# Performance work log

Measured on AMD Instinct MI355X. Metric: run time of the kernel, lower is better.

The kernel has to match this reference:

```python
import jax, jax.numpy as jnp
import numpy as np

NUM_Q = 8
B, N, D = 8, 1024, 512
C = 1024


def setup_inputs() -> dict:
    key = jax.random.key(0)
    k1, k2 = jax.random.split(key)
    x = jax.random.normal(k1, (B, N, D), dtype=jnp.float32)
    codebooks = jax.random.normal(k2, (NUM_Q, C, D), dtype=jnp.float32)
    return {"x": x, "codebooks": codebooks}


def _vq_layer(residual, codebook):
    # residual: [b, n, d]; codebook: [c, d]
    # squared euclidean distances without materializing differences tensor
    r2 = jnp.sum(residual * residual, axis=-1, keepdims=True)          # [b, n, 1]
    e2 = jnp.sum(codebook * codebook, axis=-1)                          # [c]
    dots = jnp.einsum('bnd,cd->bnc', residual, codebook)                # [b, n, c]
    dist = r2 - 2.0 * dots + e2                                         # [b, n, c]
    indices = jnp.argmin(dist, axis=-1)                                 # [b, n] int32
    quantized = codebook[indices]                                       # [b, n, d]
    # straight-through estimator (codebook is EMA-updated, not differentiated)
    quantized_st = residual + jax.lax.stop_gradient(quantized - residual)
    # commitment loss (default commitment_weight = 1.0)
    loss = jnp.mean((jax.lax.stop_gradient(quantized_st) - residual) ** 2)
    return quantized_st, indices, loss


def reference(x, codebooks):
    def step(carry, codebook):
        residual, quantized_out = carry
        quantized, indices, loss = _vq_layer(residual, codebook)
        return (residual - quantized, quantized_out + quantized), (indices, loss)

    init = (x, jnp.zeros_like(x))
    (_, quantized_out), (all_indices, all_losses) = jax.lax.scan(step, init, codebooks)
    # all_indices: [q, b, n] -> [b, n, q]; all_losses: [q]
    all_indices = jnp.transpose(all_indices, (1, 2, 0))
    return quantized_out, all_indices, all_losses
```

## Files before the change

kernel.cpp:

```cpp
#include <hip/hip_runtime.h>
#include <float.h>

#define NUM_Q 8
#define BN    8192
#define D     512
#define C     1024

#define QOUT_OFF 0
#define IDX_OFF  (BN * D)
#define LOSS_OFF (IDX_OFF + BN * NUM_Q)

#define WIN_OFF_B  0
#define E2_OFF_B   (BN * 8)

typedef _Float16 f16x8 __attribute__((ext_vector_type(8)));
typedef float    f32x4 __attribute__((ext_vector_type(4)));

#define TM  128
#define TN  128
#define BKK 32
#define LDK 40
#define GTHREADS 512

__device__ __forceinline__ unsigned fkey(float f) {
    unsigned u = __float_as_uint(f);
    return (u & 0x80000000u) ? ~u : (u | 0x80000000u);
}

__device__ __forceinline__ unsigned long long u64min(unsigned long long a, unsigned long long b) {
    return a < b ? a : b;
}

__device__ __forceinline__ unsigned long long shfl_xor_u64(unsigned long long v, int m) {
    int lo = __shfl_xor((int)(unsigned)v, m, 64);
    int hi = __shfl_xor((int)(unsigned)(v >> 32), m, 64);
    return ((unsigned long long)(unsigned)hi << 32) | (unsigned)lo;
}

__global__ void rvq_init_kernel(const float* __restrict__ x, float* __restrict__ out,
                                unsigned long long* __restrict__ winners) {
    int i = blockIdx.x * blockDim.x + threadIdx.x;
    const float4* x4 = (const float4*)x;
    float4* r4 = (float4*)(out + QOUT_OFF);
    const int n4 = BN * D / 4;
    for (int k = i; k < n4; k += gridDim.x * blockDim.x)
        r4[k] = x4[k];
    if (i < BN) winners[i] = ~0ull;
    if (i < NUM_Q) out[LOSS_OFF + i] = 0.0f;
}

__global__ void rvq_e2_kernel(const float* __restrict__ cbs, float* __restrict__ e2ws) {
    const int row = blockIdx.x;
    const int lane = threadIdx.x;
    const float* p = cbs + (size_t)row * D + lane * 8;
    float4 a = *(const float4*)p;
    float4 b = *(const float4*)(p + 4);
    float ss = a.x*a.x + a.y*a.y + a.z*a.z + a.w*a.w
             + b.x*b.x + b.y*b.y + b.z*b.z + b.w*b.w;
#pragma unroll
    for (int off = 32; off >= 1; off >>= 1) ss += __shfl_xor(ss, off, 64);
    if (lane == 0) e2ws[row] = ss;
}

__global__ __launch_bounds__(GTHREADS, 4) void rvq_score_kernel(
    const float* __restrict__ cb,
    const float* __restrict__ R,
    const float* __restrict__ e2,
    unsigned long long* __restrict__ winners)
{
    __shared__ __align__(16) _Float16 AsHi[TM][LDK];
    __shared__ __align__(16) _Float16 AsLo[TM][LDK];
    __shared__ __align__(16) _Float16 BsHi[TN][LDK];
    __shared__ __align__(16) _Float16 BsLo[TN][LDK];
    __shared__ unsigned long long part[4][TM];

    const int tid  = threadIdx.x;
    const int lane = tid & 63;
    const int wv   = tid >> 6;
    const int wm   = wv & 1;
    const int wn   = wv >> 1;
    const int lm   = lane & 15;
    const int lq   = lane >> 4;

    const int mg = blockIdx.x & 63;
    const int nb = blockIdx.x >> 6;
    const int tok0 = mg * TM;
    const int cb0  = nb * TN;

    const int srow = tid >> 2;
    const int skq  = tid & 3;

    const float* Ag = R  + (size_t)(tok0 + srow) * D + skq * 8;
    const float* Bg = cb + (size_t)(cb0  + srow) * D + skq * 8;

    f32x4 acc[4][2];
#pragma unroll
    for (int mt = 0; mt < 4; ++mt)
#pragma unroll
        for (int nt = 0; nt < 2; ++nt)
            acc[mt][nt] = (f32x4){0.f, 0.f, 0.f, 0.f};

    for (int kb = 0; kb < D / BKK; ++kb) {
        const int kc = kb * BKK;
        float4 a0 = *(const float4*)(Ag + kc);
        float4 a1 = *(const float4*)(Ag + kc + 4);
        float4 b0 = *(const float4*)(Bg + kc);
        float4 b1 = *(const float4*)(Bg + kc + 4);

        __syncthreads();

        {
            float av[8] = {a0.x, a0.y, a0.z, a0.w, a1.x, a1.y, a1.z, a1.w};
            f16x8 h, l;
#pragma unroll
            for (int i = 0; i < 8; ++i) {
                _Float16 hi = (_Float16)av[i];
                h[i] = hi;
                l[i] = (_Float16)(av[i] - (float)hi);
            }
            *(f16x8*)&AsHi[srow][skq * 8] = h;
            *(f16x8*)&AsLo[srow][skq * 8] = l;
        }
        {
            float bv[8] = {b0.x, b0.y, b0.z, b0.w, b1.x, b1.y, b1.z, b1.w};
            f16x8 h, l;
#pragma unroll
            for (int i = 0; i < 8; ++i) {
                _Float16 hi = (_Float16)bv[i];
                h[i] = hi;
                l[i] = (_Float16)(bv[i] - (float)hi);
            }
            *(f16x8*)&BsHi[srow][skq * 8] = h;
            *(f16x8*)&BsLo[srow][skq * 8] = l;
        }
        __syncthreads();

        f16x8 ah[4], al[4], bh[2], bl[2];
#pragma unroll
        for (int mt = 0; mt < 4; ++mt) {
            ah[mt] = *(const f16x8*)&AsHi[wm * 64 + mt * 16 + lm][lq * 8];
            al[mt] = *(const f16x8*)&AsLo[wm * 64 + mt * 16 + lm][lq * 8];
        }
#pragma unroll
        for (int nt = 0; nt < 2; ++nt) {
            bh[nt] = *(const f16x8*)&BsHi[wn * 32 + nt * 16 + lm][lq * 8];
            bl[nt] = *(const f16x8*)&BsLo[wn * 32 + nt * 16 + lm][lq * 8];
        }
#pragma unroll
        for (int mt = 0; mt < 4; ++mt)
#pragma unroll
            for (int nt = 0; nt < 2; ++nt)
                acc[mt][nt] = __builtin_amdgcn_mfma_f32_16x16x32_f16(ah[mt], bh[nt], acc[mt][nt], 0, 0, 0);
#pragma unroll
        for (int mt = 0; mt < 4; ++mt)
#pragma unroll
            for (int nt = 0; nt < 2; ++nt)
                acc[mt][nt] = __builtin_amdgcn_mfma_f32_16x16x32_f16(ah[mt], bl[nt], acc[mt][nt], 0, 0, 0);
#pragma unroll
        for (int mt = 0; mt < 4; ++mt)
#pragma unroll
            for (int nt = 0; nt < 2; ++nt)
                acc[mt][nt] = __builtin_amdgcn_mfma_f32_16x16x32_f16(al[mt], bh[nt], acc[mt][nt], 0, 0, 0);
    }

    const int n0 = cb0 + wn * 32 + lm;
    const float e2v0 = e2[n0];
    const float e2v1 = e2[n0 + 16];

#pragma unroll
    for (int mt = 0; mt < 4; ++mt) {
#pragma unroll
        for (int r = 0; r < 4; ++r) {
            float s0 = e2v0 - 2.0f * acc[mt][0][r];
            float s1 = e2v1 - 2.0f * acc[mt][1][r];
            unsigned long long p0 = ((unsigned long long)fkey(s0) << 32) | (unsigned)n0;
            unsigned long long p1 = ((unsigned long long)fkey(s1) << 32) | (unsigned)(n0 + 16);
            unsigned long long p = u64min(p0, p1);
#pragma unroll
            for (int off = 1; off < 16; off <<= 1)
                p = u64min(p, shfl_xor_u64(p, off));
            if (lm == 0)
                part[wn][wm * 64 + mt * 16 + lq * 4 + r] = p;
        }
    }
    __syncthreads();
    if (tid < TM) {
        unsigned long long p = part[0][tid];
        p = u64min(p, part[1][tid]);
        p = u64min(p, part[2][tid]);
        p = u64min(p, part[3][tid]);
        atomicMin(&winners[tok0 + tid], p);
    }
}

__global__ __launch_bounds__(256) void rvq_update_kernel(
    const float* __restrict__ cb, float* __restrict__ out,
    unsigned long long* __restrict__ winners, int q)
{
    __shared__ float lsum[4];
    const int tid = threadIdx.x;
    const int tl  = tid >> 4;
    const int g   = tid & 15;
    const int tok = blockIdx.x * 16 + tl;

    float* R = out + QOUT_OFF;
    unsigned long long w = winners[tok];
    const int best = (int)(unsigned)(w & 0xFFFFFFFFull);
    const float* crow = cb + (size_t)best * D;
    float* rrow = R + (size_t)tok * D;

    float ss = 0.0f;
#pragma unroll
    for (int m = 0; m < 8; ++m) {
        const int off = (m * 16 + g) * 4;
        float4 r = *(const float4*)&rrow[off];
        float4 c = *(const float4*)&crow[off];
        float4 nr = make_float4(r.x - c.x, r.y - c.y, r.z - c.z, r.w - c.w);
        *(float4*)&rrow[off] = nr;
        ss += nr.x * nr.x + nr.y * nr.y + nr.z * nr.z + nr.w * nr.w;
    }
    if (g == 0) {
        out[IDX_OFF + (size_t)tok * NUM_Q + q] = (float)best;
        winners[tok] = ~0ull;
    }
#pragma unroll
    for (int off = 32; off >= 1; off >>= 1) ss += __shfl_xor(ss, off, 64);
    if ((tid & 63) == 0) lsum[tid >> 6] = ss;
    __syncthreads();
    if (tid == 0)
        atomicAdd(out + LOSS_OFF + q, lsum[0] + lsum[1] + lsum[2] + lsum[3]);
}

__global__ void rvq_finalize_kernel(const float* __restrict__ x, float* __restrict__ out) {
    int i = blockIdx.x * blockDim.x + threadIdx.x;
    const float4* x4 = (const float4*)x;
    float4* o4 = (float4*)(out + QOUT_OFF);
    const int n4 = BN * D / 4;
    for (int k = i; k < n4; k += gridDim.x * blockDim.x) {
        float4 xv = x4[k];
        float4 rv = o4[k];
        o4[k] = make_float4(xv.x - rv.x, xv.y - rv.y, xv.z - rv.z, xv.w - rv.w);
    }
    if (i < NUM_Q) out[LOSS_OFF + i] *= (1.0f / (float)(BN * D));
}

extern "C" void kernel_launch(void* const* d_in, const int* in_sizes, int n_in,
                              void* d_out, int out_size, void* d_ws, size_t ws_size,
                              hipStream_t stream) {
    const float* x   = (const float*)d_in[0];
    const float* cbs = (const float*)d_in[1];
    float* out = (float*)d_out;
    unsigned long long* winners = (unsigned long long*)((char*)d_ws + WIN_OFF_B);
    float* e2ws = (float*)((char*)d_ws + E2_OFF_B);

    hipLaunchKernelGGL(rvq_init_kernel, dim3(1024), dim3(256), 0, stream, x, out, winners);
    hipLaunchKernelGGL(rvq_e2_kernel, dim3(NUM_Q * C), dim3(64), 0, stream, cbs, e2ws);

    float* R = out + QOUT_OFF;
    for (int q = 0; q < NUM_Q; ++q) {
        const float* cb_q = cbs + (size_t)q * C * D;
        hipLaunchKernelGGL(rvq_score_kernel, dim3((BN / TM) * (C / TN)), dim3(GTHREADS), 0, stream,
                           cb_q, R, e2ws + (size_t)q * C, winners);
        hipLaunchKernelGGL(rvq_update_kernel, dim3(BN / 16), dim3(256), 0, stream,
                           cb_q, out, winners, q);
    }
    hipLaunchKernelGGL(rvq_finalize_kernel, dim3(1024), dim3(256), 0, stream, x, out);
}
```

Baseline: 445.3 us.

## Fuse all quantizer stages into one persistent per-token-block kernel with pre-split codebooks

Replaces the per-stage score/update kernel pairs with a single kernel. Each block owns 32 tokens, keeps their residuals in registers across all eight stages, and computes the full 1024-code argmin locally, so no global winners array or atomics are needed. The codebooks are split once into fp16 hi/lo halves by a prep kernel and read straight from global or L2 by MFMA fragments, which removes per-tile conversion and the residual round-trips through memory. Only 256 blocks of 512 threads run, so GPU occupancy is lower and each block re-reads the whole codebook every stage, making L2 bandwidth the likely limit.

New measurement: 644.8 us. 1.45x slower.

```diff
diff --git a/kernel.cpp b/kernel.cpp
--- a/kernel.cpp
+++ b/kernel.cpp
@@ -1,5 +1,4 @@
 #include <hip/hip_runtime.h>
-#include <float.h>
 
 #define NUM_Q 8
 #define BN    8192
@@ -10,238 +9,202 @@
 #define IDX_OFF  (BN * D)
 #define LOSS_OFF (IDX_OFF + BN * NUM_Q)
 
-#define WIN_OFF_B  0
-#define E2_OFF_B   (BN * 8)
+#define CBP_OFF_B 0
+#define E2_OFF_B  (NUM_Q * C * 1024 * 2)
 
 typedef _Float16 f16x8 __attribute__((ext_vector_type(8)));
+typedef _Float16 f16x4 __attribute__((ext_vector_type(4)));
 typedef float    f32x4 __attribute__((ext_vector_type(4)));
-
-#define TM  128
-#define TN  128
-#define BKK 32
-#define LDK 40
-#define GTHREADS 512
 
 __device__ __forceinline__ unsigned fkey(float f) {
     unsigned u = __float_as_uint(f);
     return (u & 0x80000000u) ? ~u : (u | 0x80000000u);
 }
-
 __device__ __forceinline__ unsigned long long u64min(unsigned long long a, unsigned long long b) {
     return a < b ? a : b;
 }
-
 __device__ __forceinline__ unsigned long long shfl_xor_u64(unsigned long long v, int m) {
     int lo = __shfl_xor((int)(unsigned)v, m, 64);
     int hi = __shfl_xor((int)(unsigned)(v >> 32), m, 64);
     return ((unsigned long long)(unsigned)hi << 32) | (unsigned)lo;
 }
 
-__global__ void rvq_init_kernel(const float* __restrict__ x, float* __restrict__ out,
-                                unsigned long long* __restrict__ winners) {
-    int i = blockIdx.x * blockDim.x + threadIdx.x;
-    const float4* x4 = (const float4*)x;
-    float4* r4 = (float4*)(out + QOUT_OFF);
-    const int n4 = BN * D / 4;
-    for (int k = i; k < n4; k += gridDim.x * blockDim.x)
-        r4[k] = x4[k];
-    if (i < BN) winners[i] = ~0ull;
-    if (i < NUM_Q) out[LOSS_OFF + i] = 0.0f;
-}
-
-__global__ void rvq_e2_kernel(const float* __restrict__ cbs, float* __restrict__ e2ws) {
-    const int row = blockIdx.x;
-    const int lane = threadIdx.x;
+__global__ __launch_bounds__(256) void rvq_prep(const float* __restrict__ cbs,
+                                                _Float16* __restrict__ cbp,
+                                                float* __restrict__ e2ws,
+                                                float* __restrict__ out) {
+    const int row  = blockIdx.x * 4 + (threadIdx.x >> 6);
+    const int lane = threadIdx.x & 63;
     const float* p = cbs + (size_t)row * D + lane * 8;
     float4 a = *(const float4*)p;
     float4 b = *(const float4*)(p + 4);
-    float ss = a.x*a.x + a.y*a.y + a.z*a.z + a.w*a.w
-             + b.x*b.x + b.y*b.y + b.z*b.z + b.w*b.w;
+    float av[8] = {a.x, a.y, a.z, a.w, b.x, b.y, b.z, b.w};
+    f16x8 h, l;
+    float ss = 0.f;
+#pragma unroll
+    for (int i = 0; i < 8; ++i) {
+        _Float16 hi = (_Float16)av[i];
+        h[i] = hi;
+        l[i] = (_Float16)(av[i] - (float)hi);
+        ss += av[i] * av[i];
+    }
+    _Float16* dst = cbp + (size_t)row * 1024;
+    *(f16x8*)(dst + lane * 8)       = h;
+    *(f16x8*)(dst + 512 + lane * 8) = l;
 #pragma unroll
     for (int off = 32; off >= 1; off >>= 1) ss += __shfl_xor(ss, off, 64);
     if (lane == 0) e2ws[row] = ss;
-}
-
-__global__ __launch_bounds__(GTHREADS, 4) void rvq_score_kernel(
-    const float* __restrict__ cb,
-    const float* __restrict__ R,
-    const float* __restrict__ e2,
-    unsigned long long* __restrict__ winners)
+    if (blockIdx.x == 0 && threadIdx.x < NUM_Q) out[LOSS_OFF + threadIdx.x] = 0.0f;
+}
+
+__global__ __launch_bounds__(512, 2) void rvq_fused(
+    const float* __restrict__ x, const float* __restrict__ cbs,
+    const _Float16* __restrict__ cbp, const float* __restrict__ e2ws,
+    float* __restrict__ out)
 {
-    __shared__ __align__(16) _Float16 AsHi[TM][LDK];
-    __shared__ __align__(16) _Float16 AsLo[TM][LDK];
-    __shared__ __align__(16) _Float16 BsHi[TN][LDK];
-    __shared__ __align__(16) _Float16 BsLo[TN][LDK];
-    __shared__ unsigned long long part[4][TM];
+    __shared__ __align__(16) unsigned char smem[65536];
 
     const int tid  = threadIdx.x;
     const int lane = tid & 63;
     const int wv   = tid >> 6;
-    const int wm   = wv & 1;
-    const int wn   = wv >> 1;
     const int lm   = lane & 15;
     const int lq   = lane >> 4;
-
-    const int mg = blockIdx.x & 63;
-    const int nb = blockIdx.x >> 6;
-    const int tok0 = mg * TM;
-    const int cb0  = nb * TN;
-
-    const int srow = tid >> 2;
-    const int skq  = tid & 3;
-
-    const float* Ag = R  + (size_t)(tok0 + srow) * D + skq * 8;
-    const float* Bg = cb + (size_t)(cb0  + srow) * D + skq * 8;
-
-    f32x4 acc[4][2];
-#pragma unroll
-    for (int mt = 0; mt < 4; ++mt)
-#pragma unroll
-        for (int nt = 0; nt < 2; ++nt)
-            acc[mt][nt] = (f32x4){0.f, 0.f, 0.f, 0.f};
-
-    for (int kb = 0; kb < D / BKK; ++kb) {
-        const int kc = kb * BKK;
-        float4 a0 = *(const float4*)(Ag + kc);
-        float4 a1 = *(const float4*)(Ag + kc + 4);
-        float4 b0 = *(const float4*)(Bg + kc);
-        float4 b1 = *(const float4*)(Bg + kc + 4);
-
-        __syncthreads();
-
-        {
-            float av[8] = {a0.x, a0.y, a0.z, a0.w, a1.x, a1.y, a1.z, a1.w};
-            f16x8 h, l;
-#pragma unroll
-            for (int i = 0; i < 8; ++i) {
-                _Float16 hi = (_Float16)av[i];
-                h[i] = hi;
-                l[i] = (_Float16)(av[i] - (float)hi);
+    const int tl   = tid >> 4;
+    const int g    = tid & 15;
+    const int tok0 = blockIdx.x * 32;
+
+    auto aab = [](int row, int kbyte) -> unsigned {
+        return (((unsigned)row << 10) + (unsigned)kbyte) ^ (unsigned)((row & 7) << 4);
+    };
+
+    float4 r4[8];
+    {
+        const float* xr = x + (size_t)(tok0 + tl) * D + g * 4;
+#pragma unroll
+        for (int j = 0; j < 8; ++j) r4[j] = *(const float4*)(xr + j * 64);
+    }
+
+    unsigned long long* red = (unsigned long long*)smem;
+
+    for (int q = 0; q < NUM_Q; ++q) {
+#pragma unroll
+        for (int j = 0; j < 8; ++j) {
+            float4 v = r4[j];
+            f16x4 h, l;
+            h[0] = (_Float16)v.x; l[0] = (_Float16)(v.x - (float)h[0]);
+            h[1] = (_Float16)v.y; l[1] = (_Float16)(v.y - (float)h[1]);
+            h[2] = (_Float16)v.z; l[2] = (_Float16)(v.z - (float)h[2]);
+            h[3] = (_Float16)v.w; l[3] = (_Float16)(v.w - (float)h[3]);
+            unsigned b = aab(tl, (g * 4 + j * 64) * 2);
+            *(f16x4*)(smem + b)         = h;
+            *(f16x4*)(smem + 32768 + b) = l;
+        }
+        __syncthreads();
+
+        const _Float16* bp[8];
+#pragma unroll
+        for (int nt = 0; nt < 8; ++nt)
+            bp[nt] = cbp + (((size_t)(q * C + wv * 128 + nt * 16 + lm)) << 10) + lq * 8;
+
+        f32x4 acc[2][8];
+#pragma unroll
+        for (int mt = 0; mt < 2; ++mt)
+#pragma unroll
+            for (int nt = 0; nt < 8; ++nt)
+                acc[mt][nt] = (f32x4){0.f, 0.f, 0.f, 0.f};
+
+#pragma unroll
+        for (int kb = 0; kb < 16; ++kb) {
+            unsigned b0 = aab(lm,      kb * 64 + lq * 16);
+            unsigned b1 = aab(16 + lm, kb * 64 + lq * 16);
+            f16x8 ah0 = *(const f16x8*)(smem + b0);
+            f16x8 ah1 = *(const f16x8*)(smem + b1);
+            f16x8 al0 = *(const f16x8*)(smem + 32768 + b0);
+            f16x8 al1 = *(const f16x8*)(smem + 32768 + b1);
+#pragma unroll
+            for (int nt = 0; nt < 8; ++nt) {
+                f16x8 bh = *(const f16x8*)(bp[nt] + kb * 32);
+                f16x8 bl = *(const f16x8*)(bp[nt] + 512 + kb * 32);
+                acc[0][nt] = __builtin_amdgcn_mfma_f32_16x16x32_f16(ah0, bh, acc[0][nt], 0, 0, 0);
+                acc[1][nt] = __builtin_amdgcn_mfma_f32_16x16x32_f16(ah1, bh, acc[1][nt], 0, 0, 0);
+                acc[0][nt] = __builtin_amdgcn_mfma_f32_16x16x32_f16(ah0, bl, acc[0][nt], 0, 0, 0);
+                acc[1][nt] = __builtin_amdgcn_mfma_f32_16x16x32_f16(ah1, bl, acc[1][nt], 0, 0, 0);
+                acc[0][nt] = __builtin_amdgcn_mfma_f32_16x16x32_f16(al0, bh, acc[0][nt], 0, 0, 0);
+                acc[1][nt] = __builtin_amdgcn_mfma_f32_16x16x32_f16(al1, bh, acc[1][nt], 0, 0, 0);
             }
-            *(f16x8*)&AsHi[srow][skq * 8] = h;
-            *(f16x8*)&AsLo[srow][skq * 8] = l;
-        }
-        {
-            float bv[8] = {b0.x, b0.y, b0.z, b0.w, b1.x, b1.y, b1.z, b1.w};
-            f16x8 h, l;
-#pragma unroll
-            for (int i = 0; i < 8; ++i) {
-                _Float16 hi = (_Float16)bv[i];
-                h[i] = hi;
-                l[i] = (_Float16)(bv[i] - (float)hi);
+        }
+        __syncthreads();
+
+        const float* e2q = e2ws + q * C;
+        float e2v[8];
+#pragma unroll
+        for (int nt = 0; nt < 8; ++nt) e2v[nt] = e2q[wv * 128 + nt * 16 + lm];
+
+        unsigned long long best[2][4];
+#pragma unroll
+        for (int mt = 0; mt < 2; ++mt)
+#pragma unroll
+            for (int r = 0; r < 4; ++r) best[mt][r] = ~0ull;
+
+#pragma unroll
+        for (int mt = 0; mt < 2; ++mt)
+#pragma unroll
+            for (int nt = 0; nt < 8; ++nt) {
+                unsigned col = (unsigned)(wv * 128 + nt * 16 + lm);
+#pragma unroll
+                for (int r = 0; r < 4; ++r) {
+                    float s = e2v[nt] - 2.0f * acc[mt][nt][r];
+                    unsigned long long p = ((unsigned long long)fkey(s) << 32) | col;
+                    best[mt][r] = u64min(best[mt][r], p);
+                }
             }
-            *(f16x8*)&BsHi[srow][skq * 8] = h;
-            *(f16x8*)&BsLo[srow][skq * 8] = l;
-        }
-        __syncthreads();
-
-        f16x8 ah[4], al[4], bh[2], bl[2];
-#pragma unroll
-        for (int mt = 0; mt < 4; ++mt) {
-            ah[mt] = *(const f16x8*)&AsHi[wm * 64 + mt * 16 + lm][lq * 8];
-            al[mt] = *(const f16x8*)&AsLo[wm * 64 + mt * 16 + lm][lq * 8];
-        }
-#pragma unroll
-        for (int nt = 0; nt < 2; ++nt) {
-            bh[nt] = *(const f16x8*)&BsHi[wn * 32 + nt * 16 + lm][lq * 8];
-            bl[nt] = *(const f16x8*)&BsLo[wn * 32 + nt * 16 + lm][lq * 8];
-        }
-#pragma unroll
-        for (int mt = 0; mt < 4; ++mt)
-#pragma unroll
-            for (int nt = 0; nt < 2; ++nt)
-                acc[mt][nt] = __builtin_amdgcn_mfma_f32_16x16x32_f16(ah[mt], bh[nt], acc[mt][nt], 0, 0, 0);
-#pragma unroll
-        for (int mt = 0; mt < 4; ++mt)
-#pragma unroll
-            for (int nt = 0; nt < 2; ++nt)
-                acc[mt][nt] = __builtin_amdgcn_mfma_f32_16x16x32_f16(ah[mt], bl[nt], acc[mt][nt], 0, 0, 0);
-#pragma unroll
-        for (int mt = 0; mt < 4; ++mt)
-#pragma unroll
-            for (int nt = 0; nt < 2; ++nt)
-                acc[mt][nt] = __builtin_amdgcn_mfma_f32_16x16x32_f16(al[mt], bh[nt], acc[mt][nt], 0, 0, 0);
-    }
-
-    const int n0 = cb0 + wn * 32 + lm;
-    const float e2v0 = e2[n0];
-    const float e2v1 = e2[n0 + 16];
-
-#pragma unroll
-    for (int mt = 0; mt < 4; ++mt) {
-#pragma unroll
-        for (int r = 0; r < 4; ++r) {
-            float s0 = e2v0 - 2.0f * acc[mt][0][r];
-            float s1 = e2v1 - 2.0f * acc[mt][1][r];
-            unsigned long long p0 = ((unsigned long long)fkey(s0) << 32) | (unsigned)n0;
-            unsigned long long p1 = ((unsigned long long)fkey(s1) << 32) | (unsigned)(n0 + 16);
-            unsigned long long p = u64min(p0, p1);
-#pragma unroll
-            for (int off = 1; off < 16; off <<= 1)
-                p = u64min(p, shfl_xor_u64(p, off));
-            if (lm == 0)
-                part[wn][wm * 64 + mt * 16 + lq * 4 + r] = p;
-        }
-    }
-    __syncthreads();
-    if (tid < TM) {
-        unsigned long long p = part[0][tid];
-        p = u64min(p, part[1][tid]);
-        p = u64min(p, part[2][tid]);
-        p = u64min(p, part[3][tid]);
-        atomicMin(&winners[tok0 + tid], p);
-    }
-}
-
-__global__ __launch_bounds__(256) void rvq_update_kernel(
-    const float* __restrict__ cb, float* __restrict__ out,
-    unsigned long long* __restrict__ winners, int q)
-{
-    __shared__ float lsum[4];
-    const int tid = threadIdx.x;
-    const int tl  = tid >> 4;
-    const int g   = tid & 15;
-    const int tok = blockIdx.x * 16 + tl;
-
-    float* R = out + QOUT_OFF;
-    unsigned long long w = winners[tok];
-    const int best = (int)(unsigned)(w & 0xFFFFFFFFull);
-    const float* crow = cb + (size_t)best * D;
-    float* rrow = R + (size_t)tok * D;
-
-    float ss = 0.0f;
-#pragma unroll
-    for (int m = 0; m < 8; ++m) {
-        const int off = (m * 16 + g) * 4;
-        float4 r = *(const float4*)&rrow[off];
-        float4 c = *(const float4*)&crow[off];
-        float4 nr = make_float4(r.x - c.x, r.y - c.y, r.z - c.z, r.w - c.w);
-        *(float4*)&rrow[off] = nr;
-        ss += nr.x * nr.x + nr.y * nr.y + nr.z * nr.z + nr.w * nr.w;
-    }
-    if (g == 0) {
-        out[IDX_OFF + (size_t)tok * NUM_Q + q] = (float)best;
-        winners[tok] = ~0ull;
-    }
-#pragma unroll
-    for (int off = 32; off >= 1; off >>= 1) ss += __shfl_xor(ss, off, 64);
-    if ((tid & 63) == 0) lsum[tid >> 6] = ss;
-    __syncthreads();
-    if (tid == 0)
-        atomicAdd(out + LOSS_OFF + q, lsum[0] + lsum[1] + lsum[2] + lsum[3]);
-}
-
-__global__ void rvq_finalize_kernel(const float* __restrict__ x, float* __restrict__ out) {
-    int i = blockIdx.x * blockDim.x + threadIdx.x;
-    const float4* x4 = (const float4*)x;
-    float4* o4 = (float4*)(out + QOUT_OFF);
-    const int n4 = BN * D / 4;
-    for (int k = i; k < n4; k += gridDim.x * blockDim.x) {
-        float4 xv = x4[k];
-        float4 rv = o4[k];
-        o4[k] = make_float4(xv.x - rv.x, xv.y - rv.y, xv.z - rv.z, xv.w - rv.w);
-    }
-    if (i < NUM_Q) out[LOSS_OFF + i] *= (1.0f / (float)(BN * D));
+#pragma unroll
+        for (int mt = 0; mt < 2; ++mt)
+#pragma unroll
+            for (int r = 0; r < 4; ++r) {
+#pragma unroll
+                for (int off = 1; off < 16; off <<= 1)
+                    best[mt][r] = u64min(best[mt][r], shfl_xor_u64(best[mt][r], off));
+                if (lm == 0) red[wv * 32 + mt * 16 + lq * 4 + r] = best[mt][r];
+            }
+        __syncthreads();
+        if (tid < 32) {
+            unsigned long long p = red[tid];
+#pragma unroll
+            for (int w = 1; w < 8; ++w) p = u64min(p, red[w * 32 + tid]);
+            red[tid] = p;
+        }
+        __syncthreads();
+        const unsigned bidx = (unsigned)(red[tl] & 0xffffffffull);
+
+        const float* cw = cbs + ((size_t)q * C + bidx) * D + g * 4;
+        float ss = 0.f;
+#pragma unroll
+        for (int j = 0; j < 8; ++j) {
+            float4 c = *(const float4*)(cw + j * 64);
+            float4 v = r4[j];
+            v.x -= c.x; v.y -= c.y; v.z -= c.z; v.w -= c.w;
+            r4[j] = v;
+            ss += v.x * v.x + v.y * v.y + v.z * v.z + v.w * v.w;
+        }
+        if (g == 0) out[IDX_OFF + (size_t)(tok0 + tl) * NUM_Q + q] = (float)bidx;
+#pragma unroll
+        for (int off = 32; off >= 1; off >>= 1) ss += __shfl_xor(ss, off, 64);
+        if (lane == 0) atomicAdd(out + LOSS_OFF + q, ss * (1.0f / ((float)BN * (float)D)));
+        __syncthreads();
+    }
+
+    {
+        const float* xr = x + (size_t)(tok0 + tl) * D + g * 4;
+        float* qo = out + QOUT_OFF + (size_t)(tok0 + tl) * D + g * 4;
+#pragma unroll
+        for (int j = 0; j < 8; ++j) {
+            float4 xv = *(const float4*)(xr + j * 64);
+            float4 v  = r4[j];
+            *(float4*)(qo + j * 64) =
+                make_float4(xv.x - v.x, xv.y - v.y, xv.z - v.z, xv.w - v.w);
+        }
+    }
 }
 
 extern "C" void kernel_launch(void* const* d_in, const int* in_sizes, int n_in,
@@ -250,19 +213,9 @@
     const float* x   = (const float*)d_in[0];
     const float* cbs = (const float*)d_in[1];
     float* out = (float*)d_out;
-    unsigned long long* winners = (unsigned long long*)((char*)d_ws + WIN_OFF_B);
-    float* e2ws = (float*)((char*)d_ws + E2_OFF_B);
-
-    hipLaunchKernelGGL(rvq_init_kernel, dim3(1024), dim3(256), 0, stream, x, out, winners);
-    hipLaunchKernelGGL(rvq_e2_kernel, dim3(NUM_Q * C), dim3(64), 0, stream, cbs, e2ws);
-
-    float* R = out + QOUT_OFF;
-    for (int q = 0; q < NUM_Q; ++q) {
-        const float* cb_q = cbs + (size_t)q * C * D;
-        hipLaunchKernelGGL(rvq_score_kernel, dim3((BN / TM) * (C / TN)), dim3(GTHREADS), 0, stream,
-                           cb_q, R, e2ws + (size_t)q * C, winners);
-        hipLaunchKernelGGL(rvq_update_kernel, dim3(BN / 16), dim3(256), 0, stream,
-                           cb_q, out, winners, q);
-    }
-    hipLaunchKernelGGL(rvq_finalize_kernel, dim3(1024), dim3(256), 0, stream, x, out);
-}
+    _Float16* cbp = (_Float16*)((char*)d_ws + CBP_OFF_B);
+    float* e2ws   = (float*)((char*)d_ws + E2_OFF_B);
+
+    hipLaunchKernelGGL(rvq_prep,  dim3(NUM_Q * C / 4), dim3(256), 0, stream, cbs, cbp, e2ws, out);
+    hipLaunchKernelGGL(rvq_fused, dim3(BN / 32),       dim3(512), 0, stream, x, cbs, cbp, e2ws, out);
+}
```
